# Optimization experiments

Hardware: AMD Instinct MI355X
Metric: run time of the kernel (lower is better)

The kernel has to match this reference:

```python
import math
import jax, jax.numpy as jnp
import numpy as np

NUM_ANGLE = 8
NUM_RADIAL = 3
RADIAL_MIN = 0.08
RADIAL_MAX = 0.9
EPS = 1e-6


def _hann(n):
    # torch.hann_window(n, periodic=False)
    return 0.5 * (1.0 - jnp.cos(2.0 * jnp.pi * jnp.arange(n, dtype=jnp.float32) / (n - 1)))


def _to_luma(img):
    # img: [B, 3, H, W] -> [B, H, W]
    return 0.2989 * img[:, 0] + 0.587 * img[:, 1] + 0.114 * img[:, 2]


def _log_magnitude(img):
    x = _to_luma(img).astype(jnp.float32)  # [B, H, W]
    H, W = x.shape[-2], x.shape[-1]
    win = _hann(H)[:, None] * _hann(W)[None, :]  # [H, W]
    x = x * win
    spec = jnp.fft.fftshift(jnp.fft.fft2(x, axes=(-2, -1)), axes=(-2, -1))
    return jnp.log1p(jnp.abs(spec))  # [B, H, W]


def _polar_masks(H, W):
    y = jnp.linspace(-1.0, 1.0, H, dtype=jnp.float32)
    x = jnp.linspace(-1.0, 1.0, W, dtype=jnp.float32)
    yy, xx = jnp.meshgrid(y, x, indexing='ij')
    radius = jnp.sqrt(xx * xx + yy * yy)
    radius = radius / jnp.maximum(radius.max(), EPS)
    angle = jnp.remainder(jnp.arctan2(yy, xx), math.pi)

    r_edges = jnp.linspace(RADIAL_MIN, RADIAL_MAX, NUM_RADIAL + 1, dtype=jnp.float32)
    a_edges = jnp.linspace(0.0, math.pi, NUM_ANGLE + 1, dtype=jnp.float32)

    r0 = r_edges[:-1][:, None, None]
    r1 = r_edges[1:][:, None, None]
    rmask = (radius[None] >= r0) & (radius[None] < r1)           # [R, H, W]
    rmask = rmask.at[-1].set((radius >= r_edges[-2]) & (radius <= r_edges[-1]))

    t0 = a_edges[:-1][:, None, None]
    t1 = a_edges[1:][:, None, None]
    amask = (angle[None] >= t0) & (angle[None] < t1)             # [A, H, W]
    amask = amask.at[-1].set((angle >= a_edges[-2]) & (angle <= a_edges[-1]))

    return (rmask[:, None] & amask[None, :]).astype(jnp.float32)  # [R, A, H, W]


def _sector_energies(img):
    mag = _log_magnitude(img)                          # [B, H, W]
    masks = _polar_masks(mag.shape[-2], mag.shape[-1])  # [R, A, H, W]
    mask_sum = jnp.maximum(masks.sum(axis=(-2, -1)), EPS)        # [R, A]
    masked_sum = jnp.einsum('bhw,rahw->bra', mag, masks)         # [B, R, A]
    energies = masked_sum / mask_sum[None]
    energies = energies / jnp.maximum(energies.sum(axis=-1, keepdims=True), EPS)
    return energies


def setup_inputs() -> dict:
    key = jax.random.key(0)
    k1, k2 = jax.random.split(key)
    B, C, H, W = 16, 3, 512, 512
    prediction = jax.random.uniform(k1, (B, C, H, W), dtype=jnp.float32)
    target = jax.random.uniform(k2, (B, C, H, W), dtype=jnp.float32)
    radial_weights = jnp.array([0.5, 1.0, 1.2], dtype=jnp.float32).reshape(1, NUM_RADIAL, 1)
    return {"prediction": prediction, "target": target, "radial_weights": radial_weights}


def reference(prediction, target, radial_weights):
    pred_e = _sector_energies(prediction)   # [B, R, A]
    tgt_e = _sector_energies(target)
    diff = pred_e - tgt_e
    dist = jnp.sqrt(diff * diff + EPS)      # charbonnier
    return (dist * radial_weights).mean()
```

## Files before the change

kernel.cpp:

```cpp
#include <hip/hip_runtime.h>
#include <math.h>

#define PI_F 3.14159265358979323846f
#define TWO_PI_F 6.28318530717958647692f
#define RSQ2 0.70710678118654752440f

#define WAVE_SYNC() __asm__ volatile("s_waitcnt lgkmcnt(0)" ::: "memory")
#define LADDR(a) ((a) + ((a) >> 3))

__device__ __forceinline__ float2 cadd(float2 a, float2 b){ return make_float2(a.x+b.x, a.y+b.y); }
__device__ __forceinline__ float2 csub(float2 a, float2 b){ return make_float2(a.x-b.x, a.y-b.y); }
__device__ __forceinline__ float2 cmul(float2 a, float2 b){ return make_float2(a.x*b.x - a.y*b.y, a.x*b.y + a.y*b.x); }
__device__ __forceinline__ float2 cw1(float2 a){ return make_float2(RSQ2*(a.x+a.y), RSQ2*(a.y-a.x)); }
__device__ __forceinline__ float2 cw2(float2 a){ return make_float2(a.y, -a.x); }
__device__ __forceinline__ float2 cw3(float2 a){ return make_float2(RSQ2*(a.y-a.x), -RSQ2*(a.x+a.y)); }

__device__ __forceinline__ void dft8(float2* v){
    float2 a0=cadd(v[0],v[4]), a1=cadd(v[1],v[5]), a2=cadd(v[2],v[6]), a3=cadd(v[3],v[7]);
    float2 b0=csub(v[0],v[4]);
    float2 b1=cw1(csub(v[1],v[5]));
    float2 b2=cw2(csub(v[2],v[6]));
    float2 b3=cw3(csub(v[3],v[7]));
    float2 c0=cadd(a0,a2), c2=csub(a0,a2), c1=cadd(a1,a3), c3=cw2(csub(a1,a3));
    float2 d0=cadd(b0,b2), d2=csub(b0,b2), d1=cadd(b1,b3), d3=cw2(csub(b1,b3));
    v[0]=cadd(c0,c1); v[1]=csub(c0,c1);
    v[2]=cadd(c2,c3); v[3]=csub(c2,c3);
    v[4]=cadd(d0,d1); v[5]=csub(d0,d1);
    v[6]=cadd(d2,d3); v[7]=csub(d2,d3);
}

__device__ __forceinline__ void stage_store(float2* wl, const float2* v, float2 w1,
                                            int base, int step){
    constexpr int br[8] = {0,4,2,6,1,5,3,7};
    wl[LADDR(base)] = v[0];
    float2 p = w1;
    #pragma unroll
    for (int c = 1; c < 8; ++c) {
        wl[LADDR(base + step*c)] = cmul(v[br[c]], p);
        p = cmul(p, w1);
    }
}

__device__ __forceinline__ void stage_load(const float2* wl, float2* v, int j){
    #pragma unroll
    for (int i = 0; i < 8; ++i) v[i] = wl[LADDR(j + 64*i)];
}

__device__ __forceinline__ int sector_id(int hm, int wm) {
    const float step = 2.0f / 511.0f;
    float y = -1.0f + step * (float)hm;
    float x = -1.0f + step * (float)wm;
    float radius = sqrtf(x * x + y * y);
    float r = radius / sqrtf(2.0f);
    float a = atan2f(y, x);
    a = fmodf(a, PI_F);
    if (a < 0.0f) a += PI_F;

    const float rstep = (0.9f - 0.08f) / 3.0f;
    const float re0 = 0.08f;
    const float re1 = 0.08f + rstep;
    const float re2 = 0.08f + 2.0f * rstep;
    const float re3 = 0.9f;
    int rb;
    if      (r >= re0 && r < re1)  rb = 0;
    else if (r >= re1 && r < re2)  rb = 1;
    else if (r >= re2 && r <= re3) rb = 2;
    else return -1;

    const float astep = PI_F / 8.0f;
    int ab = 7;
    #pragma unroll
    for (int i = 0; i < 7; ++i) {
        float t0 = astep * (float)i;
        float t1 = astep * (float)(i + 1);
        if (a >= t0 && a < t1) { ab = i; break; }
    }
    return rb * 8 + ab;
}

__device__ __forceinline__ float hannf(int i) {
    return 0.5f * (1.0f - __cosf(TWO_PI_F * (float)i / 511.0f));
}

__global__ void zero_kernel(float* p, int n) {
    int i = blockIdx.x * 256 + threadIdx.x;
    if (i < n) p[i] = 0.0f;
}

__global__ __launch_bounds__(256) void rowfft_kernel(const float* __restrict__ pred,
                                                     const float* __restrict__ tgt,
                                                     float4* __restrict__ out4,
                                                     unsigned char* __restrict__ mapT,
                                                     float* __restrict__ counts) {
    __shared__ float2 lds[4 * 576];
    __shared__ float cbins[24];
    int blk = blockIdx.x;
    int img = blk >> 6;
    int pb  = blk & 63;
    int t = threadIdx.x;
    int wv = t >> 6, j = t & 63;
    int hp = pb * 4 + wv;
    int h0 = 2 * hp;
    float2* wl = lds + wv * 576;

    if (t < 24) cbins[t] = 0.0f;
    __syncthreads();
    if (t < 128) {
        int idx = blk * 128 + t;
        int wm = idx >> 9, hm = idx & 511;
        int s = sector_id(hm, wm);
        mapT[idx] = (unsigned char)(s < 0 ? 255 : s);
        if (s >= 0) atomicAdd(&cbins[s], 1.0f);
    }

    const float* base = (img < 16) ? (pred + (size_t)img * 786432)
                                   : (tgt  + (size_t)(img - 16) * 786432);
    float wh0 = hannf(h0), wh1 = hannf(h0 + 1);
    float2 v[8];
    #pragma unroll
    for (int i = 0; i < 8; ++i) {
        int w = j + 64 * i;
        float ww = hannf(w);
        size_t off0 = (size_t)h0 * 512 + w;
        size_t off1 = off0 + 512;
        float l0 = 0.2989f*base[off0] + 0.587f*base[off0+262144] + 0.114f*base[off0+524288];
        float l1 = 0.2989f*base[off1] + 0.587f*base[off1+262144] + 0.114f*base[off1+524288];
        v[i] = make_float2(l0 * (wh0 * ww), l1 * (wh1 * ww));
    }
    float sn, cs;
    dft8(v);
    __sincosf(-TWO_PI_F * (float)j / 512.0f, &sn, &cs);
    stage_store(wl, v, make_float2(cs, sn), 8 * j, 1);
    WAVE_SYNC();
    stage_load(wl, v, j);
    WAVE_SYNC();
    dft8(v);
    __sincosf(-TWO_PI_F * (float)((j >> 3) << 3) / 512.0f, &sn, &cs);
    stage_store(wl, v, make_float2(cs, sn), (j & 7) + 64 * (j >> 3), 8);
    WAVE_SYNC();
    stage_load(wl, v, j);
    dft8(v);
    constexpr int br[8] = {0,4,2,6,1,5,3,7};
    size_t kbase = (size_t)img * 257;
    int partner = (64 - j) & 63;
    #pragma unroll
    for (int c = 0; c < 4; ++c) {
        float2 zk = v[br[c]];
        float mx = __shfl(v[br[7 - c]].x, partner, 64);
        float my = __shfl(v[br[7 - c]].y, partner, 64);
        float2 zs = v[br[(8 - c) & 7]];
        float2 zm = make_float2(j == 0 ? zs.x : mx, j == 0 ? zs.y : my);
        int k = j + 64 * c;
        float4 o = make_float4(0.5f*(zk.x+zm.x), 0.5f*(zk.y-zm.y),
                               0.5f*(zk.y+zm.y), 0.5f*(zm.x-zk.x));
        out4[(kbase + k) * 256 + hp] = o;
    }
    if (j == 0) {
        float2 z = v[br[4]];
        out4[(kbase + 256) * 256 + hp] = make_float4(z.x, 0.0f, z.y, 0.0f);
    }
    __syncthreads();
    if (t < 24) {
        float c = cbins[t];
        if (c != 0.0f) atomicAdd(&counts[t], c);
    }
}

__global__ __launch_bounds__(256) void colfft_kernel(const float2* __restrict__ buf,
                                                     const unsigned char* __restrict__ mapT,
                                                     float* __restrict__ acc) {
    __shared__ float2 lds[4 * 576];
    __shared__ float bins[4 * 200];
    int t = threadIdx.x;
    int wv = t >> 6, j = t & 63;
    int gid = blockIdx.x * 4 + wv;
    int img = gid / 257;
    int w = gid - img * 257;
    float2* wl = lds + wv * 576;
    float* wb = bins + wv * 200;
    #pragma unroll
    for (int i = 0; i < 4; ++i) {
        int ii = j + 64 * i;
        if (ii < 200) wb[ii] = 0.0f;
    }
    const float2* col = buf + (size_t)gid * 512;
    float2 v[8];
    #pragma unroll
    for (int i = 0; i < 8; ++i) v[i] = col[j + 64 * i];
    float sn, cs;
    dft8(v);
    __sincosf(-TWO_PI_F * (float)j / 512.0f, &sn, &cs);
    stage_store(wl, v, make_float2(cs, sn), 8 * j, 1);
    WAVE_SYNC();
    stage_load(wl, v, j);
    WAVE_SYNC();
    dft8(v);
    __sincosf(-TWO_PI_F * (float)((j >> 3) << 3) / 512.0f, &sn, &cs);
    stage_store(wl, v, make_float2(cs, sn), (j & 7) + 64 * (j >> 3), 8);
    WAVE_SYNC();
    stage_load(wl, v, j);
    dft8(v);
    constexpr int br[8] = {0,4,2,6,1,5,3,7};
    const unsigned char* mw  = mapT + (size_t)((w + 256) & 511) * 512;
    const unsigned char* mw2 = mapT + (size_t)((256 - w) & 511) * 512;
    bool mir = (w >= 1 && w <= 255);
    int rep = (j & 7) * 25;
    #pragma unroll
    for (int c = 0; c < 8; ++c) {
        float2 z = v[br[c]];
        float mag = log1pf(sqrtf(z.x * z.x + z.y * z.y));
        int hm = j + 64 * ((c + 4) & 7);
        int s1 = mw[hm];
        if (s1 < 24) atomicAdd(&wb[rep + s1], mag);
        if (mir) {
            int hm2 = (256 - (j + 64 * c)) & 511;
            int s2 = mw2[hm2];
            if (s2 < 24) atomicAdd(&wb[rep + s2], mag);
        }
    }
    WAVE_SYNC();
    if (j < 24) {
        float sum = 0.0f;
        #pragma unroll
        for (int r = 0; r < 8; ++r) sum += wb[r * 25 + j];
        atomicAdd(&acc[img * 24 + j], sum);
    }
}

__global__ __launch_bounds__(384) void final_kernel(const float* __restrict__ acc,
                                                    const float* __restrict__ counts,
                                                    const float* __restrict__ rw,
                                                    float* __restrict__ out) {
    __shared__ float ep[384], et[384], red[384];
    int t = threadIdx.x;
    int b = t / 24;
    int s = t % 24;
    int r = s >> 3;
    float cnt = fmaxf(counts[s], 1e-6f);
    ep[t] = acc[b * 24 + s] / cnt;
    et[t] = acc[(16 + b) * 24 + s] / cnt;
    __syncthreads();
    int gbase = b * 24 + r * 8;
    float sp = 0.0f, st = 0.0f;
    #pragma unroll
    for (int a = 0; a < 8; ++a) { sp += ep[gbase + a]; st += et[gbase + a]; }
    float pe = ep[t] / fmaxf(sp, 1e-6f);
    float te = et[t] / fmaxf(st, 1e-6f);
    float d = pe - te;
    float dist = sqrtf(d * d + 1e-6f);
    red[t] = dist * rw[r];
    __syncthreads();
    if (t < 128) red[t] += red[t + 128] + red[t + 256];
    __syncthreads();
    if (t < 64) {
        float v = red[t] + red[t + 64];
        #pragma unroll
        for (int o = 32; o > 0; o >>= 1) v += __shfl_down(v, o, 64);
        if (t == 0) out[0] = v / 384.0f;
    }
}

extern "C" void kernel_launch(void* const* d_in, const int* in_sizes, int n_in,
                              void* d_out, int out_size, void* d_ws, size_t ws_size,
                              hipStream_t stream) {
    const float* pred = (const float*)d_in[0];
    const float* tgt  = (const float*)d_in[1];
    const float* rw   = (const float*)d_in[2];

    char* ws = (char*)d_ws;
    float* acc    = (float*)ws;
    float* counts = acc + 32 * 24;
    unsigned char* mapT = (unsigned char*)(ws + 4096);
    float2* buf   = (float2*)(ws + 4096 + 262144);

    zero_kernel<<<4, 256, 0, stream>>>(acc, 32 * 24 + 24);
    rowfft_kernel<<<32 * 64, 256, 0, stream>>>(pred, tgt, (float4*)buf, mapT, counts);
    colfft_kernel<<<2056, 256, 0, stream>>>(buf, mapT, acc);
    final_kernel<<<1, 384, 0, stream>>>(acc, counts, rw, (float*)d_out);
}
```

Measured before the change: 205.5 us.

## Drop zero kernel, pack Nyquist column with DC, replicate accumulators, prefetch sector maps

```diff
diff --git a/kernel.cpp b/kernel.cpp
--- a/kernel.cpp
+++ b/kernel.cpp
@@ -82,16 +82,12 @@
     return 0.5f * (1.0f - __cosf(TWO_PI_F * (float)i / 511.0f));
 }
 
-__global__ void zero_kernel(float* p, int n) {
-    int i = blockIdx.x * 256 + threadIdx.x;
-    if (i < n) p[i] = 0.0f;
-}
-
 __global__ __launch_bounds__(256) void rowfft_kernel(const float* __restrict__ pred,
                                                      const float* __restrict__ tgt,
                                                      float4* __restrict__ out4,
                                                      unsigned char* __restrict__ mapT,
-                                                     float* __restrict__ counts) {
+                                                     unsigned char* __restrict__ cnt_u8,
+                                                     float* __restrict__ acc_rep) {
     __shared__ float2 lds[4 * 576];
     __shared__ float cbins[24];
     int blk = blockIdx.x;
@@ -103,6 +99,7 @@
     int h0 = 2 * hp;
     float2* wl = lds + wv * 576;
 
+    if (blk < 48) acc_rep[blk * 256 + t] = 0.0f;
     if (t < 24) cbins[t] = 0.0f;
     __syncthreads();
     if (t < 128) {
@@ -141,7 +138,7 @@
     stage_load(wl, v, j);
     dft8(v);
     constexpr int br[8] = {0,4,2,6,1,5,3,7};
-    size_t kbase = (size_t)img * 257;
+    size_t kbase = (size_t)img * 256;
     int partner = (64 - j) & 63;
     #pragma unroll
     for (int c = 0; c < 4; ++c) {
@@ -153,40 +150,44 @@
         int k = j + 64 * c;
         float4 o = make_float4(0.5f*(zk.x+zm.x), 0.5f*(zk.y-zm.y),
                                0.5f*(zk.y+zm.y), 0.5f*(zm.x-zk.x));
-        out4[(kbase + k) * 256 + hp] = o;
+        if (k != 0) out4[(kbase + (size_t)k) * 256 + hp] = o;
     }
     if (j == 0) {
-        float2 z = v[br[4]];
-        out4[(kbase + 256) * 256 + hp] = make_float4(z.x, 0.0f, z.y, 0.0f);
-    }
-    __syncthreads();
-    if (t < 24) {
-        float c = cbins[t];
-        if (c != 0.0f) atomicAdd(&counts[t], c);
-    }
-}
-
-__global__ __launch_bounds__(256) void colfft_kernel(const float2* __restrict__ buf,
-                                                     const unsigned char* __restrict__ mapT,
-                                                     float* __restrict__ acc) {
+        float2 z0 = v[br[0]], z4 = v[br[4]];
+        out4[kbase * 256 + hp] = make_float4(z0.x, z4.x, z0.y, z4.y);
+    }
+    __syncthreads();
+    if (t < 24) cnt_u8[t * 2048 + blk] = (unsigned char)(int)cbins[t];
+}
+
+__global__ __launch_bounds__(256, 8) void colfft_kernel(const float2* __restrict__ buf,
+                                                        const unsigned char* __restrict__ mapT,
+                                                        float* __restrict__ acc_rep) {
     __shared__ float2 lds[4 * 576];
-    __shared__ float bins[4 * 200];
     int t = threadIdx.x;
     int wv = t >> 6, j = t & 63;
     int gid = blockIdx.x * 4 + wv;
-    int img = gid / 257;
-    int w = gid - img * 257;
+    int img = gid >> 8;
+    int widx = gid & 255;
     float2* wl = lds + wv * 576;
-    float* wb = bins + wv * 200;
-    #pragma unroll
-    for (int i = 0; i < 4; ++i) {
-        int ii = j + 64 * i;
-        if (ii < 200) wb[ii] = 0.0f;
-    }
+
     const float2* col = buf + (size_t)gid * 512;
     float2 v[8];
     #pragma unroll
     for (int i = 0; i < 8; ++i) v[i] = col[j + 64 * i];
+
+    bool pairw = (widx == 0);
+    const unsigned char* mwA = mapT + (size_t)(pairw ? 256 : ((widx + 256) & 511)) * 512;
+    const unsigned char* mwB = mapT + (size_t)(pairw ? 0   : ((256 - widx) & 511)) * 512;
+    unsigned char sA[8], sB[8];
+    #pragma unroll
+    for (int c = 0; c < 8; ++c) {
+        int hm = j + 64 * ((c + 4) & 7);
+        sA[c] = mwA[hm];
+        int hm2 = pairw ? hm : ((256 - (j + 64 * c)) & 511);
+        sB[c] = mwB[hm2];
+    }
+
     float sn, cs;
     dft8(v);
     __sincosf(-TWO_PI_F * (float)j / 512.0f, &sn, &cs);
@@ -200,22 +201,37 @@
     WAVE_SYNC();
     stage_load(wl, v, j);
     dft8(v);
+    WAVE_SYNC();
+    float* wb = (float*)wl;
+    #pragma unroll
+    for (int i = 0; i < 4; ++i) { int ii = j + 64 * i; if (ii < 200) wb[ii] = 0.0f; }
+    WAVE_SYNC();
+
     constexpr int br[8] = {0,4,2,6,1,5,3,7};
-    const unsigned char* mw  = mapT + (size_t)((w + 256) & 511) * 512;
-    const unsigned char* mw2 = mapT + (size_t)((256 - w) & 511) * 512;
-    bool mir = (w >= 1 && w <= 255);
     int rep = (j & 7) * 25;
-    #pragma unroll
-    for (int c = 0; c < 8; ++c) {
-        float2 z = v[br[c]];
-        float mag = log1pf(sqrtf(z.x * z.x + z.y * z.y));
-        int hm = j + 64 * ((c + 4) & 7);
-        int s1 = mw[hm];
-        if (s1 < 24) atomicAdd(&wb[rep + s1], mag);
-        if (mir) {
-            int hm2 = (256 - (j + 64 * c)) & 511;
-            int s2 = mw2[hm2];
-            if (s2 < 24) atomicAdd(&wb[rep + s2], mag);
+    if (pairw) {
+        int partner = (64 - j) & 63;
+        #pragma unroll
+        for (int c = 0; c < 8; ++c) {
+            float2 zk = v[br[c]];
+            float mx = __shfl(v[br[7 - c]].x, partner, 64);
+            float my = __shfl(v[br[7 - c]].y, partner, 64);
+            float2 zs = v[br[(8 - c) & 7]];
+            float2 zm = make_float2(j == 0 ? zs.x : mx, j == 0 ? zs.y : my);
+            float f0x = 0.5f*(zk.x+zm.x), f0y = 0.5f*(zk.y-zm.y);
+            float f1x = 0.5f*(zk.y+zm.y), f1y = 0.5f*(zm.x-zk.x);
+            float mag0 = log1pf(sqrtf(f0x*f0x + f0y*f0y));
+            float mag1 = log1pf(sqrtf(f1x*f1x + f1y*f1y));
+            int s1 = sA[c]; if (s1 < 24) atomicAdd(&wb[rep + s1], mag0);
+            int s2 = sB[c]; if (s2 < 24) atomicAdd(&wb[rep + s2], mag1);
+        }
+    } else {
+        #pragma unroll
+        for (int c = 0; c < 8; ++c) {
+            float2 z = v[br[c]];
+            float mag = log1pf(sqrtf(z.x * z.x + z.y * z.y));
+            int s1 = sA[c]; if (s1 < 24) atomicAdd(&wb[rep + s1], mag);
+            int s2 = sB[c]; if (s2 < 24) atomicAdd(&wb[rep + s2], mag);
         }
     }
     WAVE_SYNC();
@@ -223,40 +239,62 @@
         float sum = 0.0f;
         #pragma unroll
         for (int r = 0; r < 8; ++r) sum += wb[r * 25 + j];
-        atomicAdd(&acc[img * 24 + j], sum);
-    }
-}
-
-__global__ __launch_bounds__(384) void final_kernel(const float* __restrict__ acc,
-                                                    const float* __restrict__ counts,
+        atomicAdd(&acc_rep[(gid & 15) * 768 + img * 24 + j], sum);
+    }
+}
+
+__global__ __launch_bounds__(256) void final_kernel(const float* __restrict__ acc_rep,
+                                                    const unsigned char* __restrict__ cnt_u8,
                                                     const float* __restrict__ rw,
                                                     float* __restrict__ out) {
+    __shared__ float accs[768];
+    __shared__ float cnts[24];
     __shared__ float ep[384], et[384], red[384];
     int t = threadIdx.x;
-    int b = t / 24;
-    int s = t % 24;
-    int r = s >> 3;
-    float cnt = fmaxf(counts[s], 1e-6f);
-    ep[t] = acc[b * 24 + s] / cnt;
-    et[t] = acc[(16 + b) * 24 + s] / cnt;
-    __syncthreads();
-    int gbase = b * 24 + r * 8;
-    float sp = 0.0f, st = 0.0f;
-    #pragma unroll
-    for (int a = 0; a < 8; ++a) { sp += ep[gbase + a]; st += et[gbase + a]; }
-    float pe = ep[t] / fmaxf(sp, 1e-6f);
-    float te = et[t] / fmaxf(st, 1e-6f);
-    float d = pe - te;
-    float dist = sqrtf(d * d + 1e-6f);
-    red[t] = dist * rw[r];
+    for (int o = t; o < 768; o += 256) {
+        float s = 0.0f;
+        #pragma unroll
+        for (int r = 0; r < 16; ++r) s += acc_rep[r * 768 + o];
+        accs[o] = s;
+    }
+    if (t < 192) {
+        int s = t >> 3, g = t & 7;
+        const uchar4* p = (const uchar4*)(cnt_u8 + s * 2048 + g * 256);
+        float sum = 0.0f;
+        #pragma unroll
+        for (int i = 0; i < 64; ++i) { uchar4 u = p[i]; sum += (float)(u.x + u.y + u.z + u.w); }
+        sum += __shfl_down(sum, 4, 8);
+        sum += __shfl_down(sum, 2, 8);
+        sum += __shfl_down(sum, 1, 8);
+        if (g == 0) cnts[s] = sum;
+    }
+    __syncthreads();
+    for (int idx = t; idx < 384; idx += 256) {
+        int b = idx / 24, s = idx - b * 24;
+        float cnt = fmaxf(cnts[s], 1e-6f);
+        ep[idx] = accs[b * 24 + s] / cnt;
+        et[idx] = accs[(16 + b) * 24 + s] / cnt;
+    }
+    __syncthreads();
+    for (int idx = t; idx < 384; idx += 256) {
+        int b = idx / 24, s = idx - b * 24, r = s >> 3;
+        int gbase = b * 24 + r * 8;
+        float sp = 0.0f, st = 0.0f;
+        #pragma unroll
+        for (int a = 0; a < 8; ++a) { sp += ep[gbase + a]; st += et[gbase + a]; }
+        float pe = ep[idx] / fmaxf(sp, 1e-6f);
+        float te = et[idx] / fmaxf(st, 1e-6f);
+        float d = pe - te;
+        red[idx] = sqrtf(d * d + 1e-6f) * rw[r];
+    }
     __syncthreads();
     if (t < 128) red[t] += red[t + 128] + red[t + 256];
     __syncthreads();
     if (t < 64) {
-        float v = red[t] + red[t + 64];
-        #pragma unroll
-        for (int o = 32; o > 0; o >>= 1) v += __shfl_down(v, o, 64);
-        if (t == 0) out[0] = v / 384.0f;
+        float vv = red[t] + red[t + 64];
+        #pragma unroll
+        for (int o = 32; o > 0; o >>= 1) vv += __shfl_down(vv, o, 64);
+        if (t == 0) out[0] = vv / 384.0f;
     }
 }
 
@@ -268,13 +306,12 @@
     const float* rw   = (const float*)d_in[2];
 
     char* ws = (char*)d_ws;
-    float* acc    = (float*)ws;
-    float* counts = acc + 32 * 24;
-    unsigned char* mapT = (unsigned char*)(ws + 4096);
-    float2* buf   = (float2*)(ws + 4096 + 262144);
-
-    zero_kernel<<<4, 256, 0, stream>>>(acc, 32 * 24 + 24);
-    rowfft_kernel<<<32 * 64, 256, 0, stream>>>(pred, tgt, (float4*)buf, mapT, counts);
-    colfft_kernel<<<2056, 256, 0, stream>>>(buf, mapT, acc);
-    final_kernel<<<1, 384, 0, stream>>>(acc, counts, rw, (float*)d_out);
-}
+    float* acc_rep      = (float*)ws;
+    unsigned char* cnt  = (unsigned char*)(ws + 49152);
+    unsigned char* mapT = (unsigned char*)(ws + 98304);
+    float2* buf         = (float2*)(ws + 360448);
+
+    rowfft_kernel<<<2048, 256, 0, stream>>>(pred, tgt, (float4*)buf, mapT, cnt, acc_rep);
+    colfft_kernel<<<2048, 256, 0, stream>>>(buf, mapT, acc_rep);
+    final_kernel<<<1, 256, 0, stream>>>(acc_rep, cnt, rw, (float*)d_out);
+}
```

Measured after the change: 203.3 us. No clear change (-1.0%).
